# Kernel tuning notes

Hardware: AMD Instinct MI355X
Metric: run time of the kernel (lower is better)

Reference implementation:

```python
import jax, jax.numpy as jnp
import numpy as np

INTERVAL = 4
UPSCALE = 4
K = 3              # sample_size
SAMPLERS = 3
Q = 2 ** INTERVAL                 # 16
L = 2 ** (8 - INTERVAL) + 1       # 17
PAD = K - 1
B, H, W = 4, 512, 512

_STRIDES = np.array([L ** 3, L ** 2, L, 1], dtype=np.int32)


def ste_round(x):
    # straight-through round (round_func in the torch code)
    return x + jax.lax.stop_gradient(jnp.round(x) - x)


def fix_weight(w):
    return jnp.clip(ste_round(w * 127.0), -127.0, 127.0)


def sample(img, sw, sb):
    # unfold(K, K-1) + conv-per-patch + fold is exactly a VALID conv.
    # img: (B,1,h+PAD,w+PAD); sw: (4,1,K,K) -> a,b,c,d each (B,1,h,w)
    out = jax.lax.conv_general_dilated(img, sw, (1, 1), 'VALID',
        dimension_numbers=('NCHW', 'OIHW', 'NCHW')) + sb[None, :, None, None]
    return out[:, 0:1], out[:, 1:2], out[:, 2:3], out[:, 3:4]


def interp(lut, res_w, sw, sb, scale, img_in, prev_img):
    # InterpTorchBatch: 4D simplex interpolation into the quantized LUT.
    # Sorted-simplex form is equivalent to the 24-case masked torch code
    # (ties yield zero-weight terms, so tie ordering is irrelevant).
    w = fix_weight(lut)                                       # (L^4, scale*scale)
    a, b, c, d = sample(img_in, sw, sb)
    if prev_img is not None:
        rw = jnp.clip(res_w, 0.0, 1.0)
        pa, pb, pc, pd = sample(prev_img, sw, sb)
        a = rw[0, 0] * pa + (1.0 - rw[0, 0]) * a
        b = rw[0, 1] * pb + (1.0 - rw[0, 1]) * b
        c = rw[1, 0] * pc + (1.0 - rw[1, 0]) * c
        d = rw[1, 1] * pd + (1.0 - rw[1, 1]) * d
    vals = jnp.concatenate([a, b, c, d], axis=1).transpose(0, 2, 3, 1)   # (B,h,w,4)
    lo = jnp.floor_divide(vals, float(Q)).astype(jnp.int32)
    f = jnp.mod(vals, float(Q))
    order = jnp.argsort(-f, axis=-1)                          # fractional parts, descending
    fs = jnp.take_along_axis(f, order, axis=-1)
    strides = jnp.asarray(_STRIDES)
    base = jnp.sum(lo * strides, axis=-1)                     # flat index of p0000
    inc = jnp.cumsum(strides[order], axis=-1)
    verts = jnp.concatenate([base[..., None], base[..., None] + inc], axis=-1)  # (B,h,w,5)
    ws = jnp.concatenate([float(Q) - fs[..., :1], fs[..., :-1] - fs[..., 1:], fs[..., -1:]], axis=-1)
    p = w[verts]                                              # gather: (B,h,w,5,scale*scale)
    out = jnp.einsum('bhwv,bhwvk->bhwk', ws, p) / float(Q)
    bb, hh, ww, _ = out.shape
    out = out.reshape(bb, hh, ww, scale, scale).transpose(0, 1, 3, 2, 4)
    return out.reshape(bb, 1, hh * scale, ww * scale)


def _pad_rot(x, r):
    return jnp.pad(jnp.rot90(x, r, axes=(2, 3)),
                   ((0, 0), (0, 0), (0, PAD), (0, PAD)), mode='edge')


def rotate_input(lut, scale, sw, sb, x, res_w, prev_x):
    pred = jnp.zeros((), jnp.float32)
    for r in range(4):
        pr = None if prev_x is None else _pad_rot(prev_x, r)
        pred = pred + jnp.rot90(
            interp(lut, res_w, sw, sb, scale, _pad_rot(x, r), pr),
            (4 - r) % 4, axes=(2, 3))
        pred = ste_round(pred)
    return pred


def autolut_forward(x, lut0, lut1, samp0, samp1, sbias0, sbias1, resw1):
    x = x * 255.0
    # stage 0: scale 1, no residual, bias 127
    pred = 0.0
    for s in range(SAMPLERS):
        pred = pred + rotate_input(lut0[s], 1, samp0[s], sbias0[s], x, None, None)
    prev_x = x
    x = ste_round(jnp.clip(pred / (SAMPLERS * 4.0) + 127.0, 0.0, 255.0))
    # stage 1 (last): upscale, residual blend with previous stage input
    pred = 0.0
    for s in range(SAMPLERS):
        pred = pred + rotate_input(lut1[s], UPSCALE, samp1[s], sbias1[s], x, resw1[s], prev_x)
    x = ste_round(jnp.clip(pred / float(SAMPLERS), 0.0, 255.0))
    return x / 255.0   # phase == 'train'


def setup_inputs() -> dict:
    key = jax.random.key(0)
    ks = jax.random.split(key, 6)
    x = jax.random.uniform(ks[0], (B, 1, H, W), dtype=jnp.float32)
    lut0 = jax.random.uniform(ks[1], (SAMPLERS, L ** 4, 1), jnp.float32, -1.0, 1.0)
    lut1 = jax.random.uniform(ks[2], (SAMPLERS, L ** 4, UPSCALE * UPSCALE), jnp.float32, -1.0, 1.0)

    def mk_sampler(k):
        w = jax.random.normal(k, (SAMPLERS, 4, 1, K, K), dtype=jnp.float32)
        # convex combination of patch pixels -> sampled values stay in [0,255]
        return jax.nn.softmax(w.reshape(SAMPLERS, 4, -1), axis=-1).reshape(SAMPLERS, 4, 1, K, K)

    samp0 = mk_sampler(ks[3])
    samp1 = mk_sampler(ks[4])
    sbias0 = jnp.zeros((SAMPLERS, 4), jnp.float32)
    sbias1 = jnp.zeros((SAMPLERS, 4), jnp.float32)
    resw1 = jax.random.uniform(ks[5], (SAMPLERS, 2, 2), dtype=jnp.float32)
    return {"x": x, "lut0": lut0, "lut1": lut1, "samp0": samp0, "samp1": samp1,
            "sbias0": sbias0, "sbias1": sbias1, "resw1": resw1}


def reference(x, lut0, lut1, samp0, samp1, sbias0, sbias1, resw1):
    return autolut_forward(x, lut0, lut1, samp0, samp1, sbias0, sbias1, resw1)
```

## Files before the change

### kernel.cpp

```cpp
#include <hip/hip_runtime.h>
#include <math.h>

static constexpr int B_ = 4;
static constexpr int N_ = 512;
static constexpr int N4_ = 2048;
static constexpr int LUT_ROWS = 83521;
static constexpr int ST0 = 4913, ST1 = 289, ST2 = 17, ST3 = 1;

__device__ __forceinline__ float fixw(float v) {
    v = rintf(v * 127.0f);
    return fminf(fmaxf(v, -127.0f), 127.0f);
}

__global__ void fix_lut0_kernel(const float* __restrict__ in, char* __restrict__ out, int n) {
    int t = blockIdx.x * blockDim.x + threadIdx.x;
    if (t < n) out[t] = (char)(int)fixw(in[t]);
}

__global__ void fix_lut1_kernel(const float4* __restrict__ in, char4* __restrict__ out, int n4) {
    int t = blockIdx.x * blockDim.x + threadIdx.x;
    if (t < n4) {
        float4 v = in[t];
        char4 o;
        o.x = (char)(int)fixw(v.x);
        o.y = (char)(int)fixw(v.y);
        o.z = (char)(int)fixw(v.z);
        o.w = (char)(int)fixw(v.w);
        out[t] = o;
    }
}

struct Simplex {
    int v[5];
    float w[5];
};

__device__ __forceinline__ Simplex simplex4(float a, float b, float c, float d) {
    float fl0 = floorf(a * 0.0625f), fl1 = floorf(b * 0.0625f),
          fl2 = floorf(c * 0.0625f), fl3 = floorf(d * 0.0625f);
    float f[4] = { a - 16.0f * fl0, b - 16.0f * fl1, c - 16.0f * fl2, d - 16.0f * fl3 };
    int l0 = min(max((int)fl0, 0), 15);
    int l1 = min(max((int)fl1, 0), 15);
    int l2 = min(max((int)fl2, 0), 15);
    int l3 = min(max((int)fl3, 0), 15);
    int st[4] = { ST0, ST1, ST2, ST3 };
#define CSW(A, Bq) { if (f[A] < f[Bq]) { float tf = f[A]; f[A] = f[Bq]; f[Bq] = tf; \
                                         int ts = st[A]; st[A] = st[Bq]; st[Bq] = ts; } }
    CSW(0, 1) CSW(1, 2) CSW(2, 3) CSW(0, 1) CSW(1, 2) CSW(0, 1)
#undef CSW
    Simplex s;
    s.v[0] = l0 * ST0 + l1 * ST1 + l2 * ST2 + l3;
    s.v[1] = s.v[0] + st[0];
    s.v[2] = s.v[1] + st[1];
    s.v[3] = s.v[2] + st[2];
    s.v[4] = s.v[3] + st[3];
    s.w[0] = (16.0f - f[0]) * 0.0625f;
    s.w[1] = (f[0] - f[1]) * 0.0625f;
    s.w[2] = (f[1] - f[2]) * 0.0625f;
    s.w[3] = (f[2] - f[3]) * 0.0625f;
    s.w[4] = f[3] * 0.0625f;
    return s;
}

__device__ __forceinline__ bool tap_for_r(int r, int a, int c, int& di, int& dj) {
    if (r == 0) { di = a - 2; dj = c - 2; return (a >= 2) && (c >= 2); }
    if (r == 1) { di = 2 - c; dj = a - 2; return (a >= 2) && (c <= 2); }
    if (r == 2) { di = 2 - a; dj = 2 - c; return (a <= 2) && (c <= 2); }
    di = c - 2; dj = 2 - a; return (a <= 2) && (c >= 2);
}

__device__ __forceinline__ void unpack4(int w, float* o) {
    o[0] = (float)((w << 24) >> 24);
    o[1] = (float)((w << 16) >> 24);
    o[2] = (float)((w << 8) >> 24);
    o[3] = (float)(w >> 24);
}

__global__ __launch_bounds__(256) void stage0_kernel(
    const float* __restrict__ x,
    const char* __restrict__ lut0q,
    const float* __restrict__ samp0,
    const float* __restrict__ sbias0,
    float* __restrict__ x1)
{
    int tid = blockIdx.x * blockDim.x + threadIdx.x;
    if (tid >= B_ * N_ * N_) return;
    int j = tid & (N_ - 1);
    int i = (tid >> 9) & (N_ - 1);
    int b = tid >> 18;
    const float* xb = x + (size_t)b * N_ * N_;

    float pred = 0.0f;
    for (int s = 0; s < 3; ++s) {
        const float* w  = samp0 + s * 36;
        const float* sb = sbias0 + s * 4;
        const char* lut = lut0q + (size_t)s * LUT_ROWS;

        float vals[4][4];
        #pragma unroll
        for (int r = 0; r < 4; ++r)
            #pragma unroll
            for (int ch = 0; ch < 4; ++ch) vals[r][ch] = 0.0f;
        #pragma unroll
        for (int a = 0; a < 5; ++a) {
            int ri = min(max(i - 2 + a, 0), N_ - 1);
            #pragma unroll
            for (int c = 0; c < 5; ++c) {
                int ci = min(max(j - 2 + c, 0), N_ - 1);
                float px = xb[ri * N_ + ci] * 255.0f;
                #pragma unroll
                for (int r = 0; r < 4; ++r) {
                    int di, dj;
                    if (tap_for_r(r, a, c, di, dj)) {
                        #pragma unroll
                        for (int ch = 0; ch < 4; ++ch)
                            vals[r][ch] += w[ch * 9 + di * 3 + dj] * px;
                    }
                }
            }
        }

        float acc = 0.0f;
        #pragma unroll
        for (int r = 0; r < 4; ++r) {
            Simplex sx = simplex4(vals[r][0] + sb[0], vals[r][1] + sb[1],
                                  vals[r][2] + sb[2], vals[r][3] + sb[3]);
            float o = 0.0f;
            #pragma unroll
            for (int v = 0; v < 5; ++v)
                o += sx.w[v] * (float)lut[sx.v[v]];
            acc = rintf(acc + o);
        }
        pred += acc;
    }
    x1[tid] = rintf(fminf(fmaxf(pred / 12.0f + 127.0f, 0.0f), 255.0f));
}

__global__ __launch_bounds__(256) void stage1_kernel(
    const float* __restrict__ x,
    const float* __restrict__ x1,
    const char* __restrict__ lut1q,
    const float* __restrict__ samp1,
    const float* __restrict__ sbias1,
    const float* __restrict__ resw1,
    float* __restrict__ out)
{
    int tid = blockIdx.x * blockDim.x + threadIdx.x;
    if (tid >= B_ * N_ * N_) return;
    int j = tid & (N_ - 1);
    int i = (tid >> 9) & (N_ - 1);
    int b = tid >> 18;
    const float* xb  = x  + (size_t)b * N_ * N_;
    const float* x1b = x1 + (size_t)b * N_ * N_;

    float tot[16];
    #pragma unroll
    for (int k = 0; k < 16; ++k) tot[k] = 0.0f;

    for (int s = 0; s < 3; ++s) {
        const float* w  = samp1 + s * 36;
        const float* sb = sbias1 + s * 4;
        const char* lut = lut1q + (size_t)s * LUT_ROWS * 16;
        float rw[4];
        #pragma unroll
        for (int ch = 0; ch < 4; ++ch)
            rw[ch] = fminf(fmaxf(resw1[s * 4 + ch], 0.0f), 1.0f);

        float vc[4][4], vp[4][4];
        #pragma unroll
        for (int r = 0; r < 4; ++r)
            #pragma unroll
            for (int ch = 0; ch < 4; ++ch) { vc[r][ch] = 0.0f; vp[r][ch] = 0.0f; }
        #pragma unroll
        for (int a = 0; a < 5; ++a) {
            int ri = min(max(i - 2 + a, 0), N_ - 1);
            #pragma unroll
            for (int c = 0; c < 5; ++c) {
                int ci = min(max(j - 2 + c, 0), N_ - 1);
                float pc = x1b[ri * N_ + ci];
                float pp = xb[ri * N_ + ci] * 255.0f;
                #pragma unroll
                for (int r = 0; r < 4; ++r) {
                    int di, dj;
                    if (tap_for_r(r, a, c, di, dj)) {
                        #pragma unroll
                        for (int ch = 0; ch < 4; ++ch) {
                            float wt = w[ch * 9 + di * 3 + dj];
                            vc[r][ch] += wt * pc;
                            vp[r][ch] += wt * pp;
                        }
                    }
                }
            }
        }

        float acc[16];
        #pragma unroll
        for (int k = 0; k < 16; ++k) acc[k] = 0.0f;

        #pragma unroll
        for (int r = 0; r < 4; ++r) {
            float vals[4];
            #pragma unroll
            for (int ch = 0; ch < 4; ++ch)
                vals[ch] = rw[ch] * (vp[r][ch] + sb[ch])
                         + (1.0f - rw[ch]) * (vc[r][ch] + sb[ch]);
            Simplex sx = simplex4(vals[0], vals[1], vals[2], vals[3]);
            float oc[16];
            #pragma unroll
            for (int k = 0; k < 16; ++k) oc[k] = 0.0f;
            #pragma unroll
            for (int v = 0; v < 5; ++v) {
                const int4 q = *(const int4*)(lut + (size_t)sx.v[v] * 16);
                float p[16];
                unpack4(q.x, p); unpack4(q.y, p + 4);
                unpack4(q.z, p + 8); unpack4(q.w, p + 12);
                float wv = sx.w[v];
                #pragma unroll
                for (int k = 0; k < 16; ++k) oc[k] += wv * p[k];
            }
            #pragma unroll
            for (int u = 0; u < 4; ++u)
                #pragma unroll
                for (int v2 = 0; v2 < 4; ++v2) {
                    int k = 4 * u + v2;
                    int c = (r == 0) ? (4 * u + v2)
                          : (r == 1) ? (4 * (3 - v2) + u)
                          : (r == 2) ? (4 * (3 - u) + (3 - v2))
                                     : (4 * v2 + (3 - u));
                    acc[k] = rintf(acc[k] + oc[c]);
                }
        }
        #pragma unroll
        for (int k = 0; k < 16; ++k) tot[k] += acc[k];
    }

    float* ob = out + (size_t)b * N4_ * N4_ + (size_t)(i * 4) * N4_ + (j * 4);
    #pragma unroll
    for (int u = 0; u < 4; ++u) {
        float4 val;
        val.x = rintf(fminf(fmaxf(tot[4 * u + 0] / 3.0f, 0.0f), 255.0f)) * (1.0f / 255.0f);
        val.y = rintf(fminf(fmaxf(tot[4 * u + 1] / 3.0f, 0.0f), 255.0f)) * (1.0f / 255.0f);
        val.z = rintf(fminf(fmaxf(tot[4 * u + 2] / 3.0f, 0.0f), 255.0f)) * (1.0f / 255.0f);
        val.w = rintf(fminf(fmaxf(tot[4 * u + 3] / 3.0f, 0.0f), 255.0f)) * (1.0f / 255.0f);
        *(float4*)(ob + (size_t)u * N4_) = val;
    }
}

extern "C" void kernel_launch(void* const* d_in, const int* in_sizes, int n_in,
                              void* d_out, int out_size, void* d_ws, size_t ws_size,
                              hipStream_t stream) {
    const float* x      = (const float*)d_in[0];
    const float* lut0   = (const float*)d_in[1];
    const float* lut1   = (const float*)d_in[2];
    const float* samp0  = (const float*)d_in[3];
    const float* samp1  = (const float*)d_in[4];
    const float* sbias0 = (const float*)d_in[5];
    const float* sbias1 = (const float*)d_in[6];
    const float* resw1  = (const float*)d_in[7];
    float* out = (float*)d_out;
    char* ws   = (char*)d_ws;

    const int N_L0 = 3 * LUT_ROWS;
    const int N_L1 = 3 * LUT_ROWS * 16;
    size_t off_x1 = 0;
    size_t off_l0 = (size_t)B_ * N_ * N_ * sizeof(float);
    size_t off_l1 = (off_l0 + N_L0 + 15) & ~(size_t)15;

    float* x1 = (float*)(ws + off_x1);
    char* l0q = ws + off_l0;
    char* l1q = ws + off_l1;

    const int threads = 256;
    const int grid = (B_ * N_ * N_) / threads;

    fix_lut0_kernel<<<(N_L0 + threads - 1) / threads, threads, 0, stream>>>(lut0, l0q, N_L0);
    fix_lut1_kernel<<<(N_L1 / 4 + threads - 1) / threads, threads, 0, stream>>>(
        (const float4*)lut1, (char4*)l1q, N_L1 / 4);
    stage0_kernel<<<grid, threads, 0, stream>>>(x, l0q, samp0, sbias0, x1);
    stage1_kernel<<<grid, threads, 0, stream>>>(x, x1, l1q, samp1, sbias1, resw1, out);
}
```

Before: 301.7 us.

## Split stage0 across samplers with atomic accumulation and batch LUT gathers

Stage0 now launches one thread per (sampler, pixel) pair instead of looping over the three samplers per thread, and the per-sampler results are summed into x1 with atomicAdd. A separate finalize kernel applies the scale, clamp and round. The 20 LUT gathers per thread are also issued together before the weighted sum so more memory loads are in flight at once. The cost is a memset, atomics on every pixel, an extra kernel launch, and three times the 5x5 neighbourhood loads.

```diff
diff --git a/kernel.cpp b/kernel.cpp
--- a/kernel.cpp
+++ b/kernel.cpp
@@ -4,6 +4,7 @@
 static constexpr int B_ = 4;
 static constexpr int N_ = 512;
 static constexpr int N4_ = 2048;
+static constexpr int NPIX = B_ * N_ * N_;
 static constexpr int LUT_ROWS = 83521;
 static constexpr int ST0 = 4913, ST1 = 289, ST2 = 17, ST3 = 1;
 
@@ -76,64 +77,78 @@
     o[3] = (float)(w >> 24);
 }
 
-__global__ __launch_bounds__(256) void stage0_kernel(
+__global__ __launch_bounds__(256) void stage0_split_kernel(
     const float* __restrict__ x,
     const char* __restrict__ lut0q,
     const float* __restrict__ samp0,
     const float* __restrict__ sbias0,
-    float* __restrict__ x1)
+    float* __restrict__ x1acc)
 {
     int tid = blockIdx.x * blockDim.x + threadIdx.x;
-    if (tid >= B_ * N_ * N_) return;
-    int j = tid & (N_ - 1);
-    int i = (tid >> 9) & (N_ - 1);
-    int b = tid >> 18;
+    int pix = tid & (NPIX - 1);
+    int s = tid >> 20;
+    int j = pix & (N_ - 1);
+    int i = (pix >> 9) & (N_ - 1);
+    int b = pix >> 18;
     const float* xb = x + (size_t)b * N_ * N_;
-
-    float pred = 0.0f;
-    for (int s = 0; s < 3; ++s) {
-        const float* w  = samp0 + s * 36;
-        const float* sb = sbias0 + s * 4;
-        const char* lut = lut0q + (size_t)s * LUT_ROWS;
-
-        float vals[4][4];
-        #pragma unroll
-        for (int r = 0; r < 4; ++r)
-            #pragma unroll
-            for (int ch = 0; ch < 4; ++ch) vals[r][ch] = 0.0f;
-        #pragma unroll
-        for (int a = 0; a < 5; ++a) {
-            int ri = min(max(i - 2 + a, 0), N_ - 1);
-            #pragma unroll
-            for (int c = 0; c < 5; ++c) {
-                int ci = min(max(j - 2 + c, 0), N_ - 1);
-                float px = xb[ri * N_ + ci] * 255.0f;
-                #pragma unroll
-                for (int r = 0; r < 4; ++r) {
-                    int di, dj;
-                    if (tap_for_r(r, a, c, di, dj)) {
-                        #pragma unroll
-                        for (int ch = 0; ch < 4; ++ch)
-                            vals[r][ch] += w[ch * 9 + di * 3 + dj] * px;
-                    }
+    const float* w  = samp0 + s * 36;
+    const float* sb = sbias0 + s * 4;
+    const char* lut = lut0q + (size_t)s * LUT_ROWS;
+
+    float vals[4][4];
+    #pragma unroll
+    for (int r = 0; r < 4; ++r)
+        #pragma unroll
+        for (int ch = 0; ch < 4; ++ch) vals[r][ch] = 0.0f;
+    #pragma unroll
+    for (int a = 0; a < 5; ++a) {
+        int ri = min(max(i - 2 + a, 0), N_ - 1);
+        #pragma unroll
+        for (int c = 0; c < 5; ++c) {
+            int ci = min(max(j - 2 + c, 0), N_ - 1);
+            float px = xb[ri * N_ + ci] * 255.0f;
+            #pragma unroll
+            for (int r = 0; r < 4; ++r) {
+                int di, dj;
+                if (tap_for_r(r, a, c, di, dj)) {
+                    #pragma unroll
+                    for (int ch = 0; ch < 4; ++ch)
+                        vals[r][ch] += w[ch * 9 + di * 3 + dj] * px;
                 }
             }
         }
-
-        float acc = 0.0f;
-        #pragma unroll
-        for (int r = 0; r < 4; ++r) {
-            Simplex sx = simplex4(vals[r][0] + sb[0], vals[r][1] + sb[1],
-                                  vals[r][2] + sb[2], vals[r][3] + sb[3]);
-            float o = 0.0f;
-            #pragma unroll
-            for (int v = 0; v < 5; ++v)
-                o += sx.w[v] * (float)lut[sx.v[v]];
-            acc = rintf(acc + o);
-        }
-        pred += acc;
-    }
-    x1[tid] = rintf(fminf(fmaxf(pred / 12.0f + 127.0f, 0.0f), 255.0f));
+    }
+
+    int vidx[20];
+    float vw[20];
+    #pragma unroll
+    for (int r = 0; r < 4; ++r) {
+        Simplex sx = simplex4(vals[r][0] + sb[0], vals[r][1] + sb[1],
+                              vals[r][2] + sb[2], vals[r][3] + sb[3]);
+        #pragma unroll
+        for (int v = 0; v < 5; ++v) { vidx[r * 5 + v] = sx.v[v]; vw[r * 5 + v] = sx.w[v]; }
+    }
+    float pv[20];
+    #pragma unroll
+    for (int t = 0; t < 20; ++t) pv[t] = (float)lut[vidx[t]];
+
+    float acc = 0.0f;
+    #pragma unroll
+    for (int r = 0; r < 4; ++r) {
+        float o = vw[r * 5 + 0] * pv[r * 5 + 0];
+        #pragma unroll
+        for (int v = 1; v < 5; ++v) o += vw[r * 5 + v] * pv[r * 5 + v];
+        acc = rintf(acc + o);
+    }
+    atomicAdd(&x1acc[pix], acc);
+}
+
+__global__ void stage0_fin_kernel(float* __restrict__ x1) {
+    int t = blockIdx.x * blockDim.x + threadIdx.x;
+    if (t < NPIX) {
+        float pred = x1[t];
+        x1[t] = rintf(fminf(fmaxf(pred / 12.0f + 127.0f, 0.0f), 255.0f));
+    }
 }
 
 __global__ __launch_bounds__(256) void stage1_kernel(
@@ -146,7 +161,7 @@
     float* __restrict__ out)
 {
     int tid = blockIdx.x * blockDim.x + threadIdx.x;
-    if (tid >= B_ * N_ * N_) return;
+    if (tid >= NPIX) return;
     int j = tid & (N_ - 1);
     int i = (tid >> 9) & (N_ - 1);
     int b = tid >> 18;
@@ -264,7 +279,7 @@
     const int N_L0 = 3 * LUT_ROWS;
     const int N_L1 = 3 * LUT_ROWS * 16;
     size_t off_x1 = 0;
-    size_t off_l0 = (size_t)B_ * N_ * N_ * sizeof(float);
+    size_t off_l0 = (size_t)NPIX * sizeof(float);
     size_t off_l1 = (off_l0 + N_L0 + 15) & ~(size_t)15;
 
     float* x1 = (float*)(ws + off_x1);
@@ -272,11 +287,13 @@
     char* l1q = ws + off_l1;
 
     const int threads = 256;
-    const int grid = (B_ * N_ * N_) / threads;
-
+    const int grid = NPIX / threads;
+
+    hipMemsetAsync(x1, 0, (size_t)NPIX * sizeof(float), stream);
     fix_lut0_kernel<<<(N_L0 + threads - 1) / threads, threads, 0, stream>>>(lut0, l0q, N_L0);
     fix_lut1_kernel<<<(N_L1 / 4 + threads - 1) / threads, threads, 0, stream>>>(
         (const float4*)lut1, (char4*)l1q, N_L1 / 4);
-    stage0_kernel<<<grid, threads, 0, stream>>>(x, l0q, samp0, sbias0, x1);
+    stage0_split_kernel<<<3 * grid, threads, 0, stream>>>(x, l0q, samp0, sbias0, x1);
+    stage0_fin_kernel<<<grid, threads, 0, stream>>>(x1);
     stage1_kernel<<<grid, threads, 0, stream>>>(x, x1, l1q, samp1, sbias1, resw1, out);
 }
```

New measurement: 344.3 us. 1.14x slower.

## Stage lut0 per sampler into LDS and batch gathers in stage0

Applied to the files above, without the earlier changes.

Stage0 now runs 1024-thread blocks. For each sampler it copies that sampler's quantized int8 LUT (padded to 16-byte rows) into shared memory and does all 20 vertex lookups from LDS instead of global/L2 gathers. The lookups are split out so all gathers are issued before the weighted sums. The cost is an ~82KB block-wide copy repeated three times per block, extra barriers, and lower occupancy from the large LDS footprint and big blocks.

```diff
diff --git a/kernel.cpp b/kernel.cpp
--- a/kernel.cpp
+++ b/kernel.cpp
@@ -4,7 +4,9 @@
 static constexpr int B_ = 4;
 static constexpr int N_ = 512;
 static constexpr int N4_ = 2048;
+static constexpr int NPIX = B_ * N_ * N_;
 static constexpr int LUT_ROWS = 83521;
+static constexpr int SPAD = 83584;
 static constexpr int ST0 = 4913, ST1 = 289, ST2 = 17, ST3 = 1;
 
 __device__ __forceinline__ float fixw(float v) {
@@ -12,9 +14,10 @@
     return fminf(fmaxf(v, -127.0f), 127.0f);
 }
 
-__global__ void fix_lut0_kernel(const float* __restrict__ in, char* __restrict__ out, int n) {
+__global__ void fix_lut0_kernel(const float* __restrict__ in, char* __restrict__ out) {
     int t = blockIdx.x * blockDim.x + threadIdx.x;
-    if (t < n) out[t] = (char)(int)fixw(in[t]);
+    int s = blockIdx.y;
+    if (t < LUT_ROWS) out[(size_t)s * SPAD + t] = (char)(int)fixw(in[(size_t)s * LUT_ROWS + t]);
 }
 
 __global__ void fix_lut1_kernel(const float4* __restrict__ in, char4* __restrict__ out, int n4) {
@@ -76,15 +79,16 @@
     o[3] = (float)(w >> 24);
 }
 
-__global__ __launch_bounds__(256) void stage0_kernel(
+__global__ __launch_bounds__(1024) void stage0_kernel(
     const float* __restrict__ x,
     const char* __restrict__ lut0q,
     const float* __restrict__ samp0,
     const float* __restrict__ sbias0,
     float* __restrict__ x1)
 {
+    __shared__ char luts[SPAD];
+
     int tid = blockIdx.x * blockDim.x + threadIdx.x;
-    if (tid >= B_ * N_ * N_) return;
     int j = tid & (N_ - 1);
     int i = (tid >> 9) & (N_ - 1);
     int b = tid >> 18;
@@ -92,9 +96,16 @@
 
     float pred = 0.0f;
     for (int s = 0; s < 3; ++s) {
+        __syncthreads();
+        {
+            const int4* src = (const int4*)(lut0q + (size_t)s * SPAD);
+            int4* dst = (int4*)luts;
+            for (int t = threadIdx.x; t < SPAD / 16; t += 1024) dst[t] = src[t];
+        }
+        __syncthreads();
+
         const float* w  = samp0 + s * 36;
         const float* sb = sbias0 + s * 4;
-        const char* lut = lut0q + (size_t)s * LUT_ROWS;
 
         float vals[4][4];
         #pragma unroll
@@ -120,15 +131,25 @@
             }
         }
 
-        float acc = 0.0f;
+        int vidx[20];
+        float vw[20];
         #pragma unroll
         for (int r = 0; r < 4; ++r) {
             Simplex sx = simplex4(vals[r][0] + sb[0], vals[r][1] + sb[1],
                                   vals[r][2] + sb[2], vals[r][3] + sb[3]);
-            float o = 0.0f;
-            #pragma unroll
-            for (int v = 0; v < 5; ++v)
-                o += sx.w[v] * (float)lut[sx.v[v]];
+            #pragma unroll
+            for (int v = 0; v < 5; ++v) { vidx[r * 5 + v] = sx.v[v]; vw[r * 5 + v] = sx.w[v]; }
+        }
+        float pv[20];
+        #pragma unroll
+        for (int t = 0; t < 20; ++t) pv[t] = (float)luts[vidx[t]];
+
+        float acc = 0.0f;
+        #pragma unroll
+        for (int r = 0; r < 4; ++r) {
+            float o = vw[r * 5 + 0] * pv[r * 5 + 0];
+            #pragma unroll
+            for (int v = 1; v < 5; ++v) o += vw[r * 5 + v] * pv[r * 5 + v];
             acc = rintf(acc + o);
         }
         pred += acc;
@@ -146,7 +167,7 @@
     float* __restrict__ out)
 {
     int tid = blockIdx.x * blockDim.x + threadIdx.x;
-    if (tid >= B_ * N_ * N_) return;
+    if (tid >= NPIX) return;
     int j = tid & (N_ - 1);
     int i = (tid >> 9) & (N_ - 1);
     int b = tid >> 18;
@@ -261,22 +282,21 @@
     float* out = (float*)d_out;
     char* ws   = (char*)d_ws;
 
-    const int N_L0 = 3 * LUT_ROWS;
     const int N_L1 = 3 * LUT_ROWS * 16;
     size_t off_x1 = 0;
-    size_t off_l0 = (size_t)B_ * N_ * N_ * sizeof(float);
-    size_t off_l1 = (off_l0 + N_L0 + 15) & ~(size_t)15;
+    size_t off_l0 = (size_t)NPIX * sizeof(float);
+    size_t off_l1 = (off_l0 + (size_t)3 * SPAD + 15) & ~(size_t)15;
 
     float* x1 = (float*)(ws + off_x1);
     char* l0q = ws + off_l0;
     char* l1q = ws + off_l1;
 
     const int threads = 256;
-    const int grid = (B_ * N_ * N_) / threads;
-
-    fix_lut0_kernel<<<(N_L0 + threads - 1) / threads, threads, 0, stream>>>(lut0, l0q, N_L0);
+
+    dim3 g0((LUT_ROWS + threads - 1) / threads, 3);
+    fix_lut0_kernel<<<g0, threads, 0, stream>>>(lut0, l0q);
     fix_lut1_kernel<<<(N_L1 / 4 + threads - 1) / threads, threads, 0, stream>>>(
         (const float4*)lut1, (char4*)l1q, N_L1 / 4);
-    stage0_kernel<<<grid, threads, 0, stream>>>(x, l0q, samp0, sbias0, x1);
-    stage1_kernel<<<grid, threads, 0, stream>>>(x, x1, l1q, samp1, sbias1, resw1, out);
-}
+    stage0_kernel<<<NPIX / 1024, 1024, 0, stream>>>(x, l0q, samp0, sbias0, x1);
+    stage1_kernel<<<NPIX / threads, threads, 0, stream>>>(x, x1, l1q, samp1, sbias1, resw1, out);
+}
```

Result: slower. 316.6 us (+4.9%).
